# Performance work log

Hardware: AMD Instinct MI355X
Metric: run time of the kernel (lower is better)

The kernel has to match this reference:

```python
import jax, jax.numpy as jnp
import numpy as np

N_NODES = 50000
N_EDGES = 800000
IN_SIZE, HID_SIZE, OUT_SIZE = 512, 128, 64


def _graph_conv(feat, src, dst, W, b, out_norm, in_norm, activation=None):
    # DGL GraphConv with norm='both': h' = D_in^{-1/2} A D_out^{-1/2} (X W) + b
    x = feat * out_norm[:, None]          # scale by source (out-degree) norm
    x = x @ W                             # dense transform first (in >= out)
    msg = x[src]                          # gather per-edge messages [E, d]
    agg = jax.ops.segment_sum(msg, dst, num_segments=N_NODES)
    h = agg * in_norm[:, None] + b
    if activation is not None:
        h = activation(h)
    return h


def setup_inputs() -> dict:
    key = jax.random.key(0)
    k1, k2, k3, k4, k5, k6, k7 = jax.random.split(key, 7)
    features = jax.random.normal(k1, (N_NODES, IN_SIZE), dtype=jnp.float32)
    src = jax.random.randint(k2, (N_EDGES,), 0, N_NODES, dtype=jnp.int64)
    dst = jax.random.randint(k3, (N_EDGES,), 0, N_NODES, dtype=jnp.int64)
    # Glorot-style init as in dglnn.GraphConv
    W1 = jax.random.normal(k4, (IN_SIZE, HID_SIZE), dtype=jnp.float32) * (1.0 / np.sqrt(IN_SIZE))
    b1 = jnp.zeros((HID_SIZE,), dtype=jnp.float32)
    W2 = jax.random.normal(k5, (HID_SIZE, OUT_SIZE), dtype=jnp.float32) * (1.0 / np.sqrt(HID_SIZE))
    b2 = jnp.zeros((OUT_SIZE,), dtype=jnp.float32)
    return {"features": features, "W1": W1, "b1": b1, "W2": W2, "b2": b2,
            "src": src, "dst": dst}


def reference(features, W1, b1, W2, b2, src, dst):
    ones = jnp.ones((N_EDGES,), dtype=features.dtype)
    out_deg = jax.ops.segment_sum(ones, src, num_segments=N_NODES)
    in_deg = jax.ops.segment_sum(ones, dst, num_segments=N_NODES)
    out_norm = jax.lax.rsqrt(jnp.clip(out_deg, 1.0))  # deg clamped to >=1 as in DGL
    in_norm = jax.lax.rsqrt(jnp.clip(in_deg, 1.0))
    h = _graph_conv(features, src, dst, W1, b1, out_norm, in_norm, activation=jax.nn.relu)
    # dropout omitted (eval mode)
    h = _graph_conv(h, src, dst, W2, b2, out_norm, in_norm, activation=None)
    return h
```

## Files before the change

### kernel.cpp

```cpp
#include <hip/hip_runtime.h>

#define N_NODES 50000
#define IN_SIZE 512
#define HID 128
#define OUT 64
#define NB 256
#define SHIFT 7
#define NBUCK 391
#define SB 64
#define NBINS32 25000

typedef _Float16 f16x8 __attribute__((ext_vector_type(8)));
typedef _Float16 f16x4 __attribute__((ext_vector_type(4)));
typedef _Float16 f16x2 __attribute__((ext_vector_type(2)));
typedef float    f32x4 __attribute__((ext_vector_type(4)));

__device__ __forceinline__ bool detect_w(const int* p, int t, int* sh) {
    if (t < 64) {
        unsigned long long m = __ballot(p[2 * t + 1] == 0);
        if (t == 0) *sh = (m == ~0ull) ? 1 : 0;
    }
    __syncthreads();
    return *sh != 0;
}

__device__ __forceinline__ int load_idx(const void* p, int e, bool w) {
    return w ? (int)((const long long*)p)[e] : ((const int*)p)[e];
}

__global__ __launch_bounds__(256) void k_chist_wt(const void* __restrict__ dstp,
                                                  int* __restrict__ hist, int E, int EPB,
                                                  const float* __restrict__ W1, _Float16* __restrict__ W1T,
                                                  const float* __restrict__ W2, _Float16* __restrict__ W2T) {
    const int t = threadIdx.x, b = blockIdx.x;
    if (b >= NB) {
        int i = (b - NB) * 256 + t;
        if (i < IN_SIZE * HID) {
            int k = i >> 7, n = i & (HID - 1);
            W1T[(size_t)n * IN_SIZE + k] = (_Float16)W1[i];
        } else {
            int j = i - IN_SIZE * HID;
            if (j < HID * OUT) {
                int k = j >> 6, n = j & (OUT - 1);
                W2T[(size_t)n * HID + k] = (_Float16)W2[j];
            }
        }
        return;
    }
    __shared__ int bins[NBUCK];
    __shared__ int shw;
    for (int i = t; i < NBUCK; i += 256) bins[i] = 0;
    bool w = detect_w((const int*)dstp, t, &shw);
    __syncthreads();
    int eend = min(E, (b + 1) * EPB);
    for (int e = b * EPB + t; e < eend; e += 256)
        atomicAdd(&bins[load_idx(dstp, e, w) >> SHIFT], 1);
    __syncthreads();
    for (int i = t; i < NBUCK; i += 256) hist[i * NB + b] = bins[i];
}

__global__ __launch_bounds__(256) void k_srchist(const void* __restrict__ srcp,
                                                 unsigned int* __restrict__ partial, int E, int ESB) {
    __shared__ unsigned int bins[NBINS32];
    __shared__ int shw;
    const int t = threadIdx.x, b = blockIdx.x;
    for (int i = t; i < NBINS32; i += 256) bins[i] = 0;
    bool w = detect_w((const int*)srcp, t, &shw);
    __syncthreads();
    int eend = min(E, (b + 1) * ESB);
    for (int e = b * ESB + t; e < eend; e += 256) {
        int s = load_idx(srcp, e, w);
        atomicAdd(&bins[s >> 1], 1u << ((s & 1) << 4));
    }
    __syncthreads();
    for (int i = t; i < NBINS32; i += 256) partial[(size_t)b * NBINS32 + i] = bins[i];
}

__global__ __launch_bounds__(256) void k_scanA(int* __restrict__ hist, int* __restrict__ bsum) {
    __shared__ int s[256];
    const int t = threadIdx.x, g = blockIdx.x;
    int v = hist[g * NB + t];
    s[t] = v;
    __syncthreads();
    for (int off = 1; off < 256; off <<= 1) {
        int u = (t >= off) ? s[t - off] : 0;
        __syncthreads();
        s[t] += u;
        __syncthreads();
    }
    hist[g * NB + t] = s[t] - v;
    if (t == 255) bsum[g] = s[255];
}

__global__ __launch_bounds__(512) void k_scanB(const int* __restrict__ bsum, int* __restrict__ bb) {
    __shared__ int s[512];
    const int t = threadIdx.x;
    int v = (t < NBUCK) ? bsum[t] : 0;
    s[t] = v;
    __syncthreads();
    for (int off = 1; off < 512; off <<= 1) {
        int u = (t >= off) ? s[t - off] : 0;
        __syncthreads();
        s[t] += u;
        __syncthreads();
    }
    if (t <= NBUCK) bb[t] = s[t] - v;
}

__global__ __launch_bounds__(256) void k_cscatter(const void* __restrict__ srcp,
                                                  const void* __restrict__ dstp,
                                                  const int* __restrict__ hist,
                                                  const int* __restrict__ bb,
                                                  unsigned int* __restrict__ tmp,
                                                  int E, int EPB) {
    __shared__ int cur[NBUCK];
    __shared__ int shw;
    const int t = threadIdx.x, b = blockIdx.x;
    for (int i = t; i < NBUCK; i += 256) cur[i] = hist[i * NB + b] + bb[i];
    bool w = detect_w((const int*)dstp, t, &shw);
    __syncthreads();
    int eend = min(E, (b + 1) * EPB);
    for (int e = b * EPB + t; e < eend; e += 256) {
        int s = load_idx(srcp, e, w);
        int d = load_idx(dstp, e, w);
        int pos = atomicAdd(&cur[d >> SHIFT], 1);
        tmp[pos] = (unsigned int)s | ((unsigned int)(d & 127) << 16);
    }
}

__global__ __launch_bounds__(256) void k_fine(const unsigned int* __restrict__ tmp,
                                              const int* __restrict__ bb,
                                              const unsigned int* __restrict__ partial,
                                              int* __restrict__ rp,
                                              int* __restrict__ esrc,
                                              float* __restrict__ innorm,
                                              float* __restrict__ onorm) {
    __shared__ int fcnt[128];
    __shared__ int sc[128];
    __shared__ int fcur[128];
    const int t = threadIdx.x, u = blockIdx.x;
    const int e0 = bb[u], e1 = bb[u + 1];
    if (t < 128) fcnt[t] = 0;
    __syncthreads();
    for (int e = e0 + t; e < e1; e += 256)
        atomicAdd(&fcnt[tmp[e] >> 16], 1);
    if (t < 64) {
        int wd = u * 64 + t;
        if (wd < NBINS32) {
            int c0 = 0, c1 = 0;
            for (int b = 0; b < SB; ++b) {
                unsigned int v = partial[(size_t)b * NBINS32 + wd];
                c0 += (int)(v & 0xFFFFu);
                c1 += (int)(v >> 16);
            }
            if (c0 < 1) c0 = 1;
            if (c1 < 1) c1 = 1;
            onorm[2 * wd]     = 1.0f / sqrtf((float)c0);
            if (2 * wd + 1 < N_NODES) onorm[2 * wd + 1] = 1.0f / sqrtf((float)c1);
        }
    }
    __syncthreads();
    if (t < 128) sc[t] = fcnt[t];
    __syncthreads();
    for (int off = 1; off < 128; off <<= 1) {
        int v = (t < 128 && t >= off) ? sc[t - off] : 0;
        __syncthreads();
        if (t < 128) sc[t] += v;
        __syncthreads();
    }
    if (t < 128) {
        int base = e0 + sc[t] - fcnt[t];
        fcur[t] = base;
        int node = u * 128 + t;
        if (node < N_NODES) {
            rp[node] = base;
            int c = fcnt[t]; if (c < 1) c = 1;
            innorm[node] = 1.0f / sqrtf((float)c);
        }
    }
    if (u == NBUCK - 1 && t == 0) rp[N_NODES] = e1;
    __syncthreads();
    for (int e = e0 + t; e < e1; e += 256) {
        unsigned int p = tmp[e];
        int pos = atomicAdd(&fcur[p >> 16], 1);
        esrc[pos] = (int)(p & 0xFFFFu);
    }
}

#define LDA 40
__global__ __launch_bounds__(256) void k_gemm1_mfma(const float* __restrict__ A,
                                                    const _Float16* __restrict__ BT,
                                                    const float* __restrict__ onorm,
                                                    _Float16* __restrict__ X) {
    __shared__ _Float16 As[64 * LDA];
    __shared__ _Float16 Bs[128 * LDA];
    const int tid  = threadIdx.x;
    const int wave = tid >> 6, lane = tid & 63;
    const int lm = lane & 15, lq = lane >> 4;
    const int row0 = blockIdx.x * 64;

    const int ar = tid >> 2, aq = tid & 3;
    int arow = row0 + ar; if (arow >= N_NODES) arow = N_NODES - 1;
    const float* aptr = A + (size_t)arow * IN_SIZE + aq * 8;
    _Float16* asd = &As[ar * LDA + aq * 8];
    const int bn = tid >> 1, bh = tid & 1;
    const _Float16* bptr = BT + (size_t)bn * IN_SIZE + bh * 16;
    _Float16* bsd = &Bs[bn * LDA + bh * 16];

    f32x4 acc[8];
#pragma unroll
    for (int nt = 0; nt < 8; ++nt) acc[nt] = (f32x4){0.f, 0.f, 0.f, 0.f};

    for (int k0 = 0; k0 < IN_SIZE; k0 += 32) {
        float4 a0 = *(const float4*)(aptr + k0);
        float4 a1 = *(const float4*)(aptr + k0 + 4);
        f16x8  b0 = *(const f16x8*)(bptr + k0);
        f16x8  b1 = *(const f16x8*)(bptr + k0 + 8);
        f16x8 ap = {(_Float16)a0.x, (_Float16)a0.y, (_Float16)a0.z, (_Float16)a0.w,
                    (_Float16)a1.x, (_Float16)a1.y, (_Float16)a1.z, (_Float16)a1.w};
        __syncthreads();
        *(f16x8*)asd       = ap;
        *(f16x8*)bsd       = b0;
        *(f16x8*)(bsd + 8) = b1;
        __syncthreads();
        f16x8 af = *(const f16x8*)&As[(wave * 16 + lm) * LDA + lq * 8];
#pragma unroll
        for (int nt = 0; nt < 8; ++nt) {
            f16x8 bf = *(const f16x8*)&Bs[(nt * 16 + lm) * LDA + lq * 8];
            acc[nt] = __builtin_amdgcn_mfma_f32_16x16x32_f16(af, bf, acc[nt], 0, 0, 0);
        }
    }
#pragma unroll
    for (int i = 0; i < 4; ++i) {
        int row = row0 + wave * 16 + lq * 4 + i;
        if (row < N_NODES) {
            float on = onorm[row];
            _Float16* o = X + (size_t)row * HID + lm;
#pragma unroll
            for (int nt = 0; nt < 8; ++nt)
                o[nt * 16] = (_Float16)(acc[nt][i] * on);
        }
    }
}

__global__ __launch_bounds__(256) void k_agg1(const _Float16* __restrict__ X, const int* __restrict__ rp,
                                              const int* __restrict__ esrc, const float* __restrict__ innorm,
                                              const float* __restrict__ onorm, const float* __restrict__ b1,
                                              _Float16* __restrict__ H) {
    const int n = blockIdx.x * 8 + (threadIdx.x >> 5);
    const int c = (threadIdx.x & 31) << 2;
    if (n >= N_NODES) return;
    const int e0 = rp[n], e1 = rp[n + 1];
    float a0 = 0.f, a1 = 0.f, a2 = 0.f, a3 = 0.f;
    int e = e0;
    for (; e + 3 < e1; e += 4) {
        int s0 = esrc[e], s1 = esrc[e + 1], s2 = esrc[e + 2], s3 = esrc[e + 3];
        f16x4 v0 = *(const f16x4*)&X[(size_t)s0 * HID + c];
        f16x4 v1 = *(const f16x4*)&X[(size_t)s1 * HID + c];
        f16x4 v2 = *(const f16x4*)&X[(size_t)s2 * HID + c];
        f16x4 v3 = *(const f16x4*)&X[(size_t)s3 * HID + c];
        a0 += ((float)v0.x + (float)v1.x) + ((float)v2.x + (float)v3.x);
        a1 += ((float)v0.y + (float)v1.y) + ((float)v2.y + (float)v3.y);
        a2 += ((float)v0.z + (float)v1.z) + ((float)v2.z + (float)v3.z);
        a3 += ((float)v0.w + (float)v1.w) + ((float)v2.w + (float)v3.w);
    }
    for (; e < e1; ++e) {
        f16x4 v = *(const f16x4*)&X[(size_t)esrc[e] * HID + c];
        a0 += (float)v.x; a1 += (float)v.y; a2 += (float)v.z; a3 += (float)v.w;
    }
    float inn = innorm[n], on = onorm[n];
    float4 b = *(const float4*)&b1[c];
    float h0 = fmaxf(a0 * inn + b.x, 0.f) * on;
    float h1 = fmaxf(a1 * inn + b.y, 0.f) * on;
    float h2 = fmaxf(a2 * inn + b.z, 0.f) * on;
    float h3 = fmaxf(a3 * inn + b.w, 0.f) * on;
    *(f16x4*)&H[(size_t)n * HID + c] =
        (f16x4){(_Float16)h0, (_Float16)h1, (_Float16)h2, (_Float16)h3};
}

#define LDK 136
__global__ __launch_bounds__(256) void k_gemm2_mfma(const _Float16* __restrict__ Hm,
                                                    const _Float16* __restrict__ W2T,
                                                    _Float16* __restrict__ X2) {
    __shared__ _Float16 Hs[64 * LDK];
    __shared__ _Float16 Ws[64 * LDK];
    const int tid  = threadIdx.x;
    const int wave = tid >> 6, lane = tid & 63;
    const int lm = lane & 15, lq = lane >> 4;
    const int row0 = blockIdx.x * 64;

    const int r = tid >> 2, cch = (tid & 3) * 32;
    int hrow = row0 + r; if (hrow >= N_NODES) hrow = N_NODES - 1;
    const _Float16* hp = Hm + (size_t)hrow * HID + cch;
    const _Float16* wp = W2T + (size_t)r * HID + cch;
    _Float16* hd = &Hs[r * LDK + cch];
    _Float16* wd = &Ws[r * LDK + cch];
#pragma unroll
    for (int i = 0; i < 4; ++i) {
        *(f16x8*)(hd + i * 8) = *(const f16x8*)(hp + i * 8);
        *(f16x8*)(wd + i * 8) = *(const f16x8*)(wp + i * 8);
    }
    __syncthreads();

    f32x4 acc[4];
#pragma unroll
    for (int nt = 0; nt < 4; ++nt) acc[nt] = (f32x4){0.f, 0.f, 0.f, 0.f};
#pragma unroll
    for (int k0 = 0; k0 < HID; k0 += 32) {
        f16x8 af = *(const f16x8*)&Hs[(wave * 16 + lm) * LDK + k0 + lq * 8];
#pragma unroll
        for (int nt = 0; nt < 4; ++nt) {
            f16x8 bf = *(const f16x8*)&Ws[(nt * 16 + lm) * LDK + k0 + lq * 8];
            acc[nt] = __builtin_amdgcn_mfma_f32_16x16x32_f16(af, bf, acc[nt], 0, 0, 0);
        }
    }
#pragma unroll
    for (int i = 0; i < 4; ++i) {
        int row = row0 + wave * 16 + lq * 4 + i;
        if (row < N_NODES) {
            _Float16* o = X2 + (size_t)row * OUT + lm;
#pragma unroll
            for (int nt = 0; nt < 4; ++nt)
                o[nt * 16] = (_Float16)acc[nt][i];
        }
    }
}

__global__ __launch_bounds__(256) void k_agg2(const _Float16* __restrict__ X2, const int* __restrict__ rp,
                                              const int* __restrict__ esrc, const float* __restrict__ innorm,
                                              const float* __restrict__ b2, float* __restrict__ out) {
    const int n = blockIdx.x * 16 + (threadIdx.x >> 4);
    const int c = (threadIdx.x & 15) << 2;
    if (n >= N_NODES) return;
    const int e0 = rp[n], e1 = rp[n + 1];
    float a0 = 0.f, a1 = 0.f, a2 = 0.f, a3 = 0.f;
    int e = e0;
    for (; e + 3 < e1; e += 4) {
        int s0 = esrc[e], s1 = esrc[e + 1], s2 = esrc[e + 2], s3 = esrc[e + 3];
        f16x4 v0 = *(const f16x4*)&X2[(size_t)s0 * OUT + c];
        f16x4 v1 = *(const f16x4*)&X2[(size_t)s1 * OUT + c];
        f16x4 v2 = *(const f16x4*)&X2[(size_t)s2 * OUT + c];
        f16x4 v3 = *(const f16x4*)&X2[(size_t)s3 * OUT + c];
        a0 += ((float)v0.x + (float)v1.x) + ((float)v2.x + (float)v3.x);
        a1 += ((float)v0.y + (float)v1.y) + ((float)v2.y + (float)v3.y);
        a2 += ((float)v0.z + (float)v1.z) + ((float)v2.z + (float)v3.z);
        a3 += ((float)v0.w + (float)v1.w) + ((float)v2.w + (float)v3.w);
    }
    for (; e < e1; ++e) {
        f16x4 v = *(const f16x4*)&X2[(size_t)esrc[e] * OUT + c];
        a0 += (float)v.x; a1 += (float)v.y; a2 += (float)v.z; a3 += (float)v.w;
    }
    float inn = innorm[n];
    float4 b = *(const float4*)&b2[c];
    *(float4*)&out[(size_t)n * OUT + c] =
        make_float4(a0 * inn + b.x, a1 * inn + b.y, a2 * inn + b.z, a3 * inn + b.w);
}

extern "C" void kernel_launch(void* const* d_in, const int* in_sizes, int n_in,
                              void* d_out, int out_size, void* d_ws, size_t ws_size,
                              hipStream_t stream) {
    const float* feat = (const float*)d_in[0];
    const float* W1   = (const float*)d_in[1];
    const float* b1   = (const float*)d_in[2];
    const float* W2   = (const float*)d_in[3];
    const float* b2   = (const float*)d_in[4];
    const void*  srcp = (const void*)d_in[5];
    const void*  dstp = (const void*)d_in[6];
    const int    E    = in_sizes[5];
    float* out = (float*)d_out;

    char* w = (char*)d_ws;
    size_t off = 0;
    auto alloc = [&](size_t bytes) -> void* {
        off = (off + 255) & ~(size_t)255;
        void* p = w + off;
        off += bytes;
        return p;
    };
    int*   hist    = (int*)alloc((size_t)NBUCK * NB * 4);
    int*   bsum    = (int*)alloc((size_t)NBUCK * 4);
    int*   bb      = (int*)alloc((size_t)(NBUCK + 1) * 4);
    int*   rp      = (int*)alloc((size_t)(N_NODES + 1) * 4);
    unsigned int* spart = (unsigned int*)alloc((size_t)SB * NBINS32 * 4);
    unsigned int* tmp   = (unsigned int*)alloc((size_t)E * 4);
    int*   esrc    = (int*)alloc((size_t)E * 4);
    float* onorm   = (float*)alloc((size_t)N_NODES * 4);
    float* innorm  = (float*)alloc((size_t)N_NODES * 4);
    _Float16* W1T  = (_Float16*)alloc((size_t)IN_SIZE * HID * 2);
    _Float16* W2T  = (_Float16*)alloc((size_t)HID * OUT * 2);
    _Float16* X1   = (_Float16*)alloc((size_t)N_NODES * HID * 2);
    _Float16* Hbuf = (_Float16*)alloc((size_t)N_NODES * HID * 2);
    _Float16* X2   = (_Float16*)alloc((size_t)N_NODES * OUT * 2);
    (void)ws_size; (void)n_in; (void)out_size;

    const int EPB = (E + NB - 1) / NB;
    const int ESB = (E + SB - 1) / SB;
    const int WTB = (IN_SIZE * HID + HID * OUT + 255) / 256;

    k_chist_wt<<<NB + WTB, 256, 0, stream>>>(dstp, hist, E, EPB, W1, W1T, W2, W2T);
    k_srchist<<<SB, 256, 0, stream>>>(srcp, spart, E, ESB);
    k_scanA<<<NBUCK, 256, 0, stream>>>(hist, bsum);
    k_scanB<<<1, 512, 0, stream>>>(bsum, bb);
    k_cscatter<<<NB, 256, 0, stream>>>(srcp, dstp, hist, bb, tmp, E, EPB);
    k_fine<<<NBUCK, 256, 0, stream>>>(tmp, bb, spart, rp, esrc, innorm, onorm);

    k_gemm1_mfma<<<(N_NODES + 63) / 64, 256, 0, stream>>>(feat, W1T, onorm, X1);
    k_agg1<<<(N_NODES + 7) / 8, 256, 0, stream>>>(X1, rp, esrc, innorm, onorm, b1, Hbuf);
    k_gemm2_mfma<<<(N_NODES + 63) / 64, 256, 0, stream>>>(Hbuf, W2T, X2);
    k_agg2<<<(N_NODES + 15) / 16, 256, 0, stream>>>(X2, rp, esrc, innorm, b2, out);
}
```

Measured before the change: 301.6 us.

## Fuse layer-2 GEMM into agg1, merge src/dst histograms, widen gather loads

```diff
diff --git a/kernel.cpp b/kernel.cpp
--- a/kernel.cpp
+++ b/kernel.cpp
@@ -7,12 +7,10 @@
 #define NB 256
 #define SHIFT 7
 #define NBUCK 391
-#define SB 64
-#define NBINS32 25000
+#define NBINS8 12500
 
 typedef _Float16 f16x8 __attribute__((ext_vector_type(8)));
 typedef _Float16 f16x4 __attribute__((ext_vector_type(4)));
-typedef _Float16 f16x2 __attribute__((ext_vector_type(2)));
 typedef float    f32x4 __attribute__((ext_vector_type(4)));
 
 __device__ __forceinline__ bool detect_w(const int* p, int t, int* sh) {
@@ -28,10 +26,13 @@
     return w ? (int)((const long long*)p)[e] : ((const int*)p)[e];
 }
 
-__global__ __launch_bounds__(256) void k_chist_wt(const void* __restrict__ dstp,
-                                                  int* __restrict__ hist, int E, int EPB,
-                                                  const float* __restrict__ W1, _Float16* __restrict__ W1T,
-                                                  const float* __restrict__ W2, _Float16* __restrict__ W2T) {
+__global__ __launch_bounds__(256) void k_hist_wt(const void* __restrict__ srcp,
+                                                 const void* __restrict__ dstp,
+                                                 int* __restrict__ hist,
+                                                 unsigned int* __restrict__ spart,
+                                                 int E, int EPB,
+                                                 const float* __restrict__ W1, _Float16* __restrict__ W1T,
+                                                 const float* __restrict__ W2, _Float16* __restrict__ W2T) {
     const int t = threadIdx.x, b = blockIdx.x;
     if (b >= NB) {
         int i = (b - NB) * 256 + t;
@@ -47,33 +48,23 @@
         }
         return;
     }
-    __shared__ int bins[NBUCK];
+    __shared__ unsigned int sbins[NBINS8];
+    __shared__ int dbins[NBUCK];
     __shared__ int shw;
-    for (int i = t; i < NBUCK; i += 256) bins[i] = 0;
+    for (int i = t; i < NBINS8; i += 256) sbins[i] = 0;
+    for (int i = t; i < NBUCK; i += 256) dbins[i] = 0;
     bool w = detect_w((const int*)dstp, t, &shw);
     __syncthreads();
     int eend = min(E, (b + 1) * EPB);
-    for (int e = b * EPB + t; e < eend; e += 256)
-        atomicAdd(&bins[load_idx(dstp, e, w) >> SHIFT], 1);
-    __syncthreads();
-    for (int i = t; i < NBUCK; i += 256) hist[i * NB + b] = bins[i];
-}
-
-__global__ __launch_bounds__(256) void k_srchist(const void* __restrict__ srcp,
-                                                 unsigned int* __restrict__ partial, int E, int ESB) {
-    __shared__ unsigned int bins[NBINS32];
-    __shared__ int shw;
-    const int t = threadIdx.x, b = blockIdx.x;
-    for (int i = t; i < NBINS32; i += 256) bins[i] = 0;
-    bool w = detect_w((const int*)srcp, t, &shw);
-    __syncthreads();
-    int eend = min(E, (b + 1) * ESB);
-    for (int e = b * ESB + t; e < eend; e += 256) {
+    for (int e = b * EPB + t; e < eend; e += 256) {
         int s = load_idx(srcp, e, w);
-        atomicAdd(&bins[s >> 1], 1u << ((s & 1) << 4));
-    }
-    __syncthreads();
-    for (int i = t; i < NBINS32; i += 256) partial[(size_t)b * NBINS32 + i] = bins[i];
+        int d = load_idx(dstp, e, w);
+        atomicAdd(&dbins[d >> SHIFT], 1);
+        atomicAdd(&sbins[s >> 2], 1u << ((s & 3) << 3));
+    }
+    __syncthreads();
+    for (int i = t; i < NBUCK; i += 256) hist[i * NB + b] = dbins[i];
+    for (int i = t; i < NBINS8; i += 256) spart[(size_t)b * NBINS8 + i] = sbins[i];
 }
 
 __global__ __launch_bounds__(256) void k_scanA(int* __restrict__ hist, int* __restrict__ bsum) {
@@ -138,28 +129,46 @@
     __shared__ int fcnt[128];
     __shared__ int sc[128];
     __shared__ int fcur[128];
+    __shared__ int rs[256][4];
     const int t = threadIdx.x, u = blockIdx.x;
     const int e0 = bb[u], e1 = bb[u + 1];
     if (t < 128) fcnt[t] = 0;
     __syncthreads();
     for (int e = e0 + t; e < e1; e += 256)
         atomicAdd(&fcnt[tmp[e] >> 16], 1);
-    if (t < 64) {
-        int wd = u * 64 + t;
-        if (wd < NBINS32) {
-            int c0 = 0, c1 = 0;
-            for (int b = 0; b < SB; ++b) {
-                unsigned int v = partial[(size_t)b * NBINS32 + wd];
-                c0 += (int)(v & 0xFFFFu);
-                c1 += (int)(v >> 16);
+    {
+        const int wrd = t & 31, grp = t >> 5;
+        const int wd = u * 32 + wrd;
+        int c0 = 0, c1 = 0, c2 = 0, c3 = 0;
+        if (wd < NBINS8) {
+            for (int b = grp * 32; b < grp * 32 + 32; ++b) {
+                unsigned int v = partial[(size_t)b * NBINS8 + wd];
+                c0 += (int)(v & 255u);
+                c1 += (int)((v >> 8) & 255u);
+                c2 += (int)((v >> 16) & 255u);
+                c3 += (int)(v >> 24);
             }
-            if (c0 < 1) c0 = 1;
-            if (c1 < 1) c1 = 1;
-            onorm[2 * wd]     = 1.0f / sqrtf((float)c0);
-            if (2 * wd + 1 < N_NODES) onorm[2 * wd + 1] = 1.0f / sqrtf((float)c1);
-        }
-    }
-    __syncthreads();
+        }
+        rs[t][0] = c0; rs[t][1] = c1; rs[t][2] = c2; rs[t][3] = c3;
+    }
+    __syncthreads();
+    if (t < 32) {
+        const int wd = u * 32 + t;
+        if (wd < NBINS8) {
+            int d0 = 0, d1 = 0, d2 = 0, d3 = 0;
+            for (int g = 0; g < 8; ++g) {
+                d0 += rs[g * 32 + t][0]; d1 += rs[g * 32 + t][1];
+                d2 += rs[g * 32 + t][2]; d3 += rs[g * 32 + t][3];
+            }
+            if (d0 < 1) d0 = 1; if (d1 < 1) d1 = 1;
+            if (d2 < 1) d2 = 1; if (d3 < 1) d3 = 1;
+            int n0 = 4 * wd;
+            if (n0     < N_NODES) onorm[n0]     = 1.0f / sqrtf((float)d0);
+            if (n0 + 1 < N_NODES) onorm[n0 + 1] = 1.0f / sqrtf((float)d1);
+            if (n0 + 2 < N_NODES) onorm[n0 + 2] = 1.0f / sqrtf((float)d2);
+            if (n0 + 3 < N_NODES) onorm[n0 + 3] = 1.0f / sqrtf((float)d3);
+        }
+    }
     if (t < 128) sc[t] = fcnt[t];
     __syncthreads();
     for (int off = 1; off < 128; off <<= 1) {
@@ -243,117 +252,94 @@
     }
 }
 
-__global__ __launch_bounds__(256) void k_agg1(const _Float16* __restrict__ X, const int* __restrict__ rp,
-                                              const int* __restrict__ esrc, const float* __restrict__ innorm,
-                                              const float* __restrict__ onorm, const float* __restrict__ b1,
-                                              _Float16* __restrict__ H) {
-    const int n = blockIdx.x * 8 + (threadIdx.x >> 5);
-    const int c = (threadIdx.x & 31) << 2;
-    if (n >= N_NODES) return;
+#define LDH 136
+__global__ __launch_bounds__(256) void k_agg1_fused(const _Float16* __restrict__ X, const int* __restrict__ rp,
+                                                    const int* __restrict__ esrc, const float* __restrict__ innorm,
+                                                    const float* __restrict__ onorm, const float* __restrict__ b1,
+                                                    const _Float16* __restrict__ W2T, _Float16* __restrict__ X2) {
+    __shared__ _Float16 Hs[16 * LDH];
+    const int t = threadIdx.x;
+    const int ln = t >> 4;
+    const int c  = (t & 15) << 3;
+    const int n  = blockIdx.x * 16 + ln;
     const int e0 = rp[n], e1 = rp[n + 1];
-    float a0 = 0.f, a1 = 0.f, a2 = 0.f, a3 = 0.f;
+    float a[8] = {0.f, 0.f, 0.f, 0.f, 0.f, 0.f, 0.f, 0.f};
     int e = e0;
     for (; e + 3 < e1; e += 4) {
         int s0 = esrc[e], s1 = esrc[e + 1], s2 = esrc[e + 2], s3 = esrc[e + 3];
-        f16x4 v0 = *(const f16x4*)&X[(size_t)s0 * HID + c];
-        f16x4 v1 = *(const f16x4*)&X[(size_t)s1 * HID + c];
-        f16x4 v2 = *(const f16x4*)&X[(size_t)s2 * HID + c];
-        f16x4 v3 = *(const f16x4*)&X[(size_t)s3 * HID + c];
-        a0 += ((float)v0.x + (float)v1.x) + ((float)v2.x + (float)v3.x);
-        a1 += ((float)v0.y + (float)v1.y) + ((float)v2.y + (float)v3.y);
-        a2 += ((float)v0.z + (float)v1.z) + ((float)v2.z + (float)v3.z);
-        a3 += ((float)v0.w + (float)v1.w) + ((float)v2.w + (float)v3.w);
+        f16x8 v0 = *(const f16x8*)&X[(size_t)s0 * HID + c];
+        f16x8 v1 = *(const f16x8*)&X[(size_t)s1 * HID + c];
+        f16x8 v2 = *(const f16x8*)&X[(size_t)s2 * HID + c];
+        f16x8 v3 = *(const f16x8*)&X[(size_t)s3 * HID + c];
+#pragma unroll
+        for (int j = 0; j < 8; ++j)
+            a[j] += ((float)v0[j] + (float)v1[j]) + ((float)v2[j] + (float)v3[j]);
     }
     for (; e < e1; ++e) {
-        f16x4 v = *(const f16x4*)&X[(size_t)esrc[e] * HID + c];
-        a0 += (float)v.x; a1 += (float)v.y; a2 += (float)v.z; a3 += (float)v.w;
-    }
-    float inn = innorm[n], on = onorm[n];
-    float4 b = *(const float4*)&b1[c];
-    float h0 = fmaxf(a0 * inn + b.x, 0.f) * on;
-    float h1 = fmaxf(a1 * inn + b.y, 0.f) * on;
-    float h2 = fmaxf(a2 * inn + b.z, 0.f) * on;
-    float h3 = fmaxf(a3 * inn + b.w, 0.f) * on;
-    *(f16x4*)&H[(size_t)n * HID + c] =
-        (f16x4){(_Float16)h0, (_Float16)h1, (_Float16)h2, (_Float16)h3};
-}
-
-#define LDK 136
-__global__ __launch_bounds__(256) void k_gemm2_mfma(const _Float16* __restrict__ Hm,
-                                                    const _Float16* __restrict__ W2T,
-                                                    _Float16* __restrict__ X2) {
-    __shared__ _Float16 Hs[64 * LDK];
-    __shared__ _Float16 Ws[64 * LDK];
-    const int tid  = threadIdx.x;
-    const int wave = tid >> 6, lane = tid & 63;
+        f16x8 v = *(const f16x8*)&X[(size_t)esrc[e] * HID + c];
+#pragma unroll
+        for (int j = 0; j < 8; ++j) a[j] += (float)v[j];
+    }
+    const float inn = innorm[n], on = onorm[n];
+    float4 bA = *(const float4*)&b1[c];
+    float4 bB = *(const float4*)&b1[c + 4];
+    const float bv[8] = {bA.x, bA.y, bA.z, bA.w, bB.x, bB.y, bB.z, bB.w};
+    f16x8 h;
+#pragma unroll
+    for (int j = 0; j < 8; ++j)
+        h[j] = (_Float16)(fmaxf(a[j] * inn + bv[j], 0.f) * on);
+    *(f16x8*)&Hs[ln * LDH + c] = h;
+    __syncthreads();
+
+    const int wave = t >> 6, lane = t & 63;
     const int lm = lane & 15, lq = lane >> 4;
-    const int row0 = blockIdx.x * 64;
-
-    const int r = tid >> 2, cch = (tid & 3) * 32;
-    int hrow = row0 + r; if (hrow >= N_NODES) hrow = N_NODES - 1;
-    const _Float16* hp = Hm + (size_t)hrow * HID + cch;
-    const _Float16* wp = W2T + (size_t)r * HID + cch;
-    _Float16* hd = &Hs[r * LDK + cch];
-    _Float16* wd = &Ws[r * LDK + cch];
+    f32x4 acc = (f32x4){0.f, 0.f, 0.f, 0.f};
+#pragma unroll
+    for (int k0 = 0; k0 < HID; k0 += 32) {
+        f16x8 af = *(const f16x8*)&Hs[lm * LDH + k0 + lq * 8];
+        f16x8 bf = *(const f16x8*)&W2T[(size_t)(wave * 16 + lm) * HID + k0 + lq * 8];
+        acc = __builtin_amdgcn_mfma_f32_16x16x32_f16(af, bf, acc, 0, 0, 0);
+    }
+    const int n0 = blockIdx.x * 16;
 #pragma unroll
     for (int i = 0; i < 4; ++i) {
-        *(f16x8*)(hd + i * 8) = *(const f16x8*)(hp + i * 8);
-        *(f16x8*)(wd + i * 8) = *(const f16x8*)(wp + i * 8);
-    }
-    __syncthreads();
-
-    f32x4 acc[4];
-#pragma unroll
-    for (int nt = 0; nt < 4; ++nt) acc[nt] = (f32x4){0.f, 0.f, 0.f, 0.f};
-#pragma unroll
-    for (int k0 = 0; k0 < HID; k0 += 32) {
-        f16x8 af = *(const f16x8*)&Hs[(wave * 16 + lm) * LDK + k0 + lq * 8];
-#pragma unroll
-        for (int nt = 0; nt < 4; ++nt) {
-            f16x8 bf = *(const f16x8*)&Ws[(nt * 16 + lm) * LDK + k0 + lq * 8];
-            acc[nt] = __builtin_amdgcn_mfma_f32_16x16x32_f16(af, bf, acc[nt], 0, 0, 0);
-        }
-    }
-#pragma unroll
-    for (int i = 0; i < 4; ++i) {
-        int row = row0 + wave * 16 + lq * 4 + i;
-        if (row < N_NODES) {
-            _Float16* o = X2 + (size_t)row * OUT + lm;
-#pragma unroll
-            for (int nt = 0; nt < 4; ++nt)
-                o[nt * 16] = (_Float16)acc[nt][i];
-        }
+        int row = n0 + lq * 4 + i;
+        X2[(size_t)row * OUT + wave * 16 + lm] = (_Float16)acc[i];
     }
 }
 
 __global__ __launch_bounds__(256) void k_agg2(const _Float16* __restrict__ X2, const int* __restrict__ rp,
                                               const int* __restrict__ esrc, const float* __restrict__ innorm,
                                               const float* __restrict__ b2, float* __restrict__ out) {
-    const int n = blockIdx.x * 16 + (threadIdx.x >> 4);
-    const int c = (threadIdx.x & 15) << 2;
+    const int n = blockIdx.x * 32 + (threadIdx.x >> 3);
+    const int c = (threadIdx.x & 7) << 3;
     if (n >= N_NODES) return;
     const int e0 = rp[n], e1 = rp[n + 1];
-    float a0 = 0.f, a1 = 0.f, a2 = 0.f, a3 = 0.f;
+    float a[8] = {0.f, 0.f, 0.f, 0.f, 0.f, 0.f, 0.f, 0.f};
     int e = e0;
     for (; e + 3 < e1; e += 4) {
         int s0 = esrc[e], s1 = esrc[e + 1], s2 = esrc[e + 2], s3 = esrc[e + 3];
-        f16x4 v0 = *(const f16x4*)&X2[(size_t)s0 * OUT + c];
-        f16x4 v1 = *(const f16x4*)&X2[(size_t)s1 * OUT + c];
-        f16x4 v2 = *(const f16x4*)&X2[(size_t)s2 * OUT + c];
-        f16x4 v3 = *(const f16x4*)&X2[(size_t)s3 * OUT + c];
-        a0 += ((float)v0.x + (float)v1.x) + ((float)v2.x + (float)v3.x);
-        a1 += ((float)v0.y + (float)v1.y) + ((float)v2.y + (float)v3.y);
-        a2 += ((float)v0.z + (float)v1.z) + ((float)v2.z + (float)v3.z);
-        a3 += ((float)v0.w + (float)v1.w) + ((float)v2.w + (float)v3.w);
+        f16x8 v0 = *(const f16x8*)&X2[(size_t)s0 * OUT + c];
+        f16x8 v1 = *(const f16x8*)&X2[(size_t)s1 * OUT + c];
+        f16x8 v2 = *(const f16x8*)&X2[(size_t)s2 * OUT + c];
+        f16x8 v3 = *(const f16x8*)&X2[(size_t)s3 * OUT + c];
+#pragma unroll
+        for (int j = 0; j < 8; ++j)
+            a[j] += ((float)v0[j] + (float)v1[j]) + ((float)v2[j] + (float)v3[j]);
     }
     for (; e < e1; ++e) {
-        f16x4 v = *(const f16x4*)&X2[(size_t)esrc[e] * OUT + c];
-        a0 += (float)v.x; a1 += (float)v.y; a2 += (float)v.z; a3 += (float)v.w;
-    }
-    float inn = innorm[n];
-    float4 b = *(const float4*)&b2[c];
-    *(float4*)&out[(size_t)n * OUT + c] =
-        make_float4(a0 * inn + b.x, a1 * inn + b.y, a2 * inn + b.z, a3 * inn + b.w);
+        f16x8 v = *(const f16x8*)&X2[(size_t)esrc[e] * OUT + c];
+#pragma unroll
+        for (int j = 0; j < 8; ++j) a[j] += (float)v[j];
+    }
+    const float inn = innorm[n];
+    float4 bA = *(const float4*)&b2[c];
+    float4 bB = *(const float4*)&b2[c + 4];
+    float* o = out + (size_t)n * OUT + c;
+    *(float4*)o       = make_float4(a[0] * inn + bA.x, a[1] * inn + bA.y,
+                                    a[2] * inn + bA.z, a[3] * inn + bA.w);
+    *(float4*)(o + 4) = make_float4(a[4] * inn + bB.x, a[5] * inn + bB.y,
+                                    a[6] * inn + bB.z, a[7] * inn + bB.w);
 }
 
 extern "C" void kernel_launch(void* const* d_in, const int* in_sizes, int n_in,
@@ -381,7 +367,7 @@
     int*   bsum    = (int*)alloc((size_t)NBUCK * 4);
     int*   bb      = (int*)alloc((size_t)(NBUCK + 1) * 4);
     int*   rp      = (int*)alloc((size_t)(N_NODES + 1) * 4);
-    unsigned int* spart = (unsigned int*)alloc((size_t)SB * NBINS32 * 4);
+    unsigned int* spart = (unsigned int*)alloc((size_t)NB * NBINS8 * 4);
     unsigned int* tmp   = (unsigned int*)alloc((size_t)E * 4);
     int*   esrc    = (int*)alloc((size_t)E * 4);
     float* onorm   = (float*)alloc((size_t)N_NODES * 4);
@@ -389,23 +375,19 @@
     _Float16* W1T  = (_Float16*)alloc((size_t)IN_SIZE * HID * 2);
     _Float16* W2T  = (_Float16*)alloc((size_t)HID * OUT * 2);
     _Float16* X1   = (_Float16*)alloc((size_t)N_NODES * HID * 2);
-    _Float16* Hbuf = (_Float16*)alloc((size_t)N_NODES * HID * 2);
     _Float16* X2   = (_Float16*)alloc((size_t)N_NODES * OUT * 2);
     (void)ws_size; (void)n_in; (void)out_size;
 
     const int EPB = (E + NB - 1) / NB;
-    const int ESB = (E + SB - 1) / SB;
     const int WTB = (IN_SIZE * HID + HID * OUT + 255) / 256;
 
-    k_chist_wt<<<NB + WTB, 256, 0, stream>>>(dstp, hist, E, EPB, W1, W1T, W2, W2T);
-    k_srchist<<<SB, 256, 0, stream>>>(srcp, spart, E, ESB);
+    k_hist_wt<<<NB + WTB, 256, 0, stream>>>(srcp, dstp, hist, spart, E, EPB, W1, W1T, W2, W2T);
     k_scanA<<<NBUCK, 256, 0, stream>>>(hist, bsum);
     k_scanB<<<1, 512, 0, stream>>>(bsum, bb);
     k_cscatter<<<NB, 256, 0, stream>>>(srcp, dstp, hist, bb, tmp, E, EPB);
     k_fine<<<NBUCK, 256, 0, stream>>>(tmp, bb, spart, rp, esrc, innorm, onorm);
 
     k_gemm1_mfma<<<(N_NODES + 63) / 64, 256, 0, stream>>>(feat, W1T, onorm, X1);
-    k_agg1<<<(N_NODES + 7) / 8, 256, 0, stream>>>(X1, rp, esrc, innorm, onorm, b1, Hbuf);
-    k_gemm2_mfma<<<(N_NODES + 63) / 64, 256, 0, stream>>>(Hbuf, W2T, X2);
-    k_agg2<<<(N_NODES + 15) / 16, 256, 0, stream>>>(X2, rp, esrc, innorm, b2, out);
-}
+    k_agg1_fused<<<(N_NODES + 15) / 16, 256, 0, stream>>>(X1, rp, esrc, innorm, onorm, b1, W2T, X2);
+    k_agg2<<<(N_NODES + 31) / 32, 256, 0, stream>>>(X2, rp, esrc, innorm, b2, out);
+}
```

Result: faster. 275.9 us (-8.5%).
